# Optimization experiments

Hardware: AMD Instinct MI355X
Metric: run time of the kernel (lower is better)

The kernel has to match this reference:

```python
import jax, jax.numpy as jnp
import numpy as np

DIM = 2048
N_HEADS = 16
Q_LORA = 1536
KV_LORA = 512
NOPE = 128
ROPE = 64
QK_D = NOPE + ROPE  # 192
V_D = 128
EPS = 1e-6
B, S = 2, 2048


def rmsnorm(x, w, eps=EPS):
    return x * jax.lax.rsqrt(jnp.mean(x * x, axis=-1, keepdims=True) + eps) * w


def rotate_pe(x, cos, sin):
    # x: [B, S, H, ROPE]; cos/sin: [S, ROPE] -> broadcast [1, S, 1, ROPE]
    c = cos[None, :, None, :]
    s = sin[None, :, None, :]
    x1, x2 = jnp.split(x, 2, axis=-1)
    rot = jnp.concatenate([-x2, x1], axis=-1)
    return x * c + rot * s


def setup_inputs() -> dict:
    key = jax.random.key(0)
    ks = jax.random.split(key, 8)
    std = 0.02
    x = jax.random.normal(ks[0], (B, S, DIM), dtype=jnp.float32)
    # proper rotary tables
    inv_freq = 1.0 / (10000.0 ** (np.arange(0, ROPE, 2, dtype=np.float32) / ROPE))
    t = np.arange(S, dtype=np.float32)
    freqs = np.outer(t, inv_freq)  # [S, ROPE/2]
    emb = np.concatenate([freqs, freqs], axis=-1)  # [S, ROPE]
    cos = jnp.asarray(np.cos(emb))
    sin = jnp.asarray(np.sin(emb))
    wq_a = jax.random.normal(ks[1], (Q_LORA, DIM), dtype=jnp.float32) * std
    q_norm_w = jnp.ones((Q_LORA,), dtype=jnp.float32)
    wq_b = jax.random.normal(ks[2], (N_HEADS * QK_D, Q_LORA), dtype=jnp.float32) * std
    wkv_a = jax.random.normal(ks[3], (KV_LORA + ROPE, DIM), dtype=jnp.float32) * std
    kv_norm_w = jnp.ones((KV_LORA,), dtype=jnp.float32)
    wkv_b = jax.random.normal(ks[4], (N_HEADS * (NOPE + V_D), KV_LORA), dtype=jnp.float32) * std
    wo = jax.random.normal(ks[5], (DIM, N_HEADS * V_D), dtype=jnp.float32) * std
    return {"x": x, "cos": cos, "sin": sin, "wq_a": wq_a, "q_norm_w": q_norm_w,
            "wq_b": wq_b, "wkv_a": wkv_a, "kv_norm_w": kv_norm_w, "wkv_b": wkv_b, "wo": wo}


def mla_forward(x, cos, sin, wq_a, q_norm_w, wq_b, wkv_a, kv_norm_w, wkv_b, wo):
    bsz, seqlen, _ = x.shape
    scale = QK_D ** (-0.5)
    # Q path: low-rank down-proj -> RMSNorm -> up-proj
    q = rmsnorm(x @ wq_a.T, q_norm_w) @ wq_b.T
    q = q.reshape(bsz, seqlen, N_HEADS, QK_D)
    q_nope, q_pe = q[..., :NOPE], q[..., NOPE:]
    q_pe = rotate_pe(q_pe, cos, sin)
    q = jnp.concatenate([q_nope, q_pe], axis=-1)
    # KV path: shared low-rank latent + single rope slice
    kv = x @ wkv_a.T  # [B, S, KV_LORA + ROPE]
    kv_c, k_pe = kv[..., :KV_LORA], kv[..., KV_LORA:]
    k_pe = rotate_pe(k_pe[:, :, None, :], cos, sin)  # [B, S, 1, ROPE]
    kvb = rmsnorm(kv_c, kv_norm_w) @ wkv_b.T
    kvb = kvb.reshape(bsz, seqlen, N_HEADS, NOPE + V_D)
    k_nope, v = kvb[..., :NOPE], kvb[..., NOPE:]
    k = jnp.concatenate([k_nope, jnp.broadcast_to(k_pe, (bsz, seqlen, N_HEADS, ROPE))], axis=-1)
    # causal attention
    scores = jnp.einsum('bqhd,bkhd->bhqk', q, k) * scale
    mask = jnp.tril(jnp.ones((seqlen, seqlen), dtype=bool))
    scores = jnp.where(mask[None, None], scores, jnp.finfo(scores.dtype).min)
    p = jax.nn.softmax(scores, axis=-1)
    out = jnp.einsum('bhqk,bkhd->bqhd', p, v)
    out = out.reshape(bsz, seqlen, N_HEADS * V_D)
    return out @ wo.T


def reference(x, cos, sin, wq_a, q_norm_w, wq_b, wkv_a, kv_norm_w, wkv_b, wo):
    return mla_forward(x, cos, sin, wq_a, q_norm_w, wq_b, wkv_a, kv_norm_w, wkv_b, wo)
```

## Files before the change

kernel.cpp:

```cpp
#include <hip/hip_runtime.h>

typedef unsigned short u16;
typedef __attribute__((ext_vector_type(8))) short short8;
typedef __attribute__((ext_vector_type(4))) float floatx4;

__device__ __forceinline__ float bf2f(u16 u) {
  union { unsigned int i; float f; } v; v.i = ((unsigned int)u) << 16; return v.f;
}
__device__ __forceinline__ u16 f2bf(float f) {
  union { float f; unsigned int i; } v; v.f = f;
  unsigned int u = v.i;
  u += 0x7fffu + ((u >> 16) & 1u);
  return (u16)(u >> 16);
}

__device__ __forceinline__ void gld_lds16(const void* g, void* l) {
  __builtin_amdgcn_global_load_lds(
      (const __attribute__((address_space(1))) unsigned int*)g,
      (__attribute__((address_space(3))) unsigned int*)l, 16, 0, 0);
}

#define SBAR()   __builtin_amdgcn_s_barrier()
#define SCHED0() __builtin_amdgcn_sched_barrier(0)

__global__ __launch_bounds__(256) void repack_all_k(
    const float* __restrict__ x, const float* __restrict__ wqa,
    const float* __restrict__ wkva, const float* __restrict__ wqb,
    const float* __restrict__ wkvb, const float* __restrict__ wo,
    u16* __restrict__ xb, u16* __restrict__ wcat, u16* __restrict__ wqbb,
    u16* __restrict__ wkbb, u16* __restrict__ wob) {
  long i = ((long)blockIdx.x * 256 + threadIdx.x) * 4;
  int region = blockIdx.y;
  const float* s = nullptr; u16* d = nullptr; long n = 0;
  switch (region) {
    case 0: s = x;    d = xb;   n = 4096L * 2048; break;
    case 1: s = nullptr; d = wcat; n = 2304L * 2048; break;
    case 2: s = wqb;  d = wqbb; n = 3072L * 1536; break;
    case 3: s = wkvb; d = wkbb; n = 4096L * 512;  break;
    case 4: s = wo;   d = wob;  n = 2048L * 2048; break;
  }
  if (i >= n) return;
  float4 v;
  if (region == 1) {
    long r = i >> 11, c = i & 2047;
    if (r < 1536)      v = *(const float4*)(wqa + r * 2048 + c);
    else if (r < 2112) v = *(const float4*)(wkva + (r - 1536) * 2048 + c);
    else               v = (float4){0.f, 0.f, 0.f, 0.f};
  } else {
    v = *(const float4*)(s + i);
  }
  d[i + 0] = f2bf(v.x); d[i + 1] = f2bf(v.y);
  d[i + 2] = f2bf(v.z); d[i + 3] = f2bf(v.w);
}

#define GPHASE(LAc, LBc, QQ, STAGE_STMT, WAIT_STMT)                              \
  {                                                                              \
    short8 a00 = *(const short8*)&(LAc)[agbase + (2*(QQ)) * 1024 + g0];          \
    short8 a01 = *(const short8*)&(LAc)[agbase + (2*(QQ)) * 1024 + g1];          \
    short8 a10 = *(const short8*)&(LAc)[agbase + (2*(QQ)+1) * 1024 + g0];        \
    short8 a11 = *(const short8*)&(LAc)[agbase + (2*(QQ)+1) * 1024 + g1];        \
    if ((QQ) == 0) {                                                             \
      _Pragma("unroll")                                                          \
      for (int fj = 0; fj < 4; ++fj) {                                           \
        bfrg[fj][0] = *(const short8*)&(LBc)[bgbase + fj * 1024 + g0];           \
        bfrg[fj][1] = *(const short8*)&(LBc)[bgbase + fj * 1024 + g1];           \
      }                                                                          \
    }                                                                            \
    STAGE_STMT;                                                                  \
    WAIT_STMT;                                                                   \
    SCHED0();                                                                    \
    SBAR();                                                                      \
    asm volatile("s_waitcnt lgkmcnt(0)" ::: "memory");                           \
    SCHED0();                                                                    \
    __builtin_amdgcn_s_setprio(1);                                               \
    _Pragma("unroll")                                                            \
    for (int fj = 0; fj < 4; ++fj) {                                             \
      acc[2*(QQ)][fj]   = __builtin_amdgcn_mfma_f32_16x16x32_bf16(a00, bfrg[fj][0], acc[2*(QQ)][fj],   0, 0, 0); \
      acc[2*(QQ)][fj]   = __builtin_amdgcn_mfma_f32_16x16x32_bf16(a01, bfrg[fj][1], acc[2*(QQ)][fj],   0, 0, 0); \
      acc[2*(QQ)+1][fj] = __builtin_amdgcn_mfma_f32_16x16x32_bf16(a10, bfrg[fj][0], acc[2*(QQ)+1][fj], 0, 0, 0); \
      acc[2*(QQ)+1][fj] = __builtin_amdgcn_mfma_f32_16x16x32_bf16(a11, bfrg[fj][1], acc[2*(QQ)+1][fj], 0, 0, 0); \
    }                                                                            \
    __builtin_amdgcn_s_setprio(0);                                               \
    SCHED0();                                                                    \
    SBAR();                                                                      \
  }

template <int OUT_F32, int ROPE>
__device__ __forceinline__ void gemm256_tile(
    const u16* __restrict__ A, int lda, const u16* __restrict__ W, int ldw,
    void* __restrict__ Cv, int ldc, int K, int bm, int bn,
    u16* __restrict__ LA, u16* __restrict__ LB,
    const float* __restrict__ cosb, const float* __restrict__ sinb, int smask) {
  int tid = threadIdx.x;
  int lane = tid & 63, w = tid >> 6;
  int wr = w >> 2, wc = w & 3;
  int fr = lane & 15, fq = lane >> 4;

  int srow = lane >> 3;
  int sgl  = (lane & 7) ^ srow;

  int agbase = (wr * 128 + fr) * 64;
  int bgbase = (wc * 64 + fr) * 64;
  int g0 = ((0 * 4 + fq) ^ (fr & 7)) * 8;
  int g1 = ((1 * 4 + fq) ^ (fr & 7)) * 8;

  floatx4 acc[8][4];
#pragma unroll
  for (int i = 0; i < 8; i++)
#pragma unroll
    for (int j = 0; j < 4; j++) acc[i][j] = (floatx4){0.f, 0.f, 0.f, 0.f};

  auto stA = [&](int buf, int kt, int half) {
#pragma unroll
    for (int j = 0; j < 2; ++j) {
      int rbase = half * 128 + (w * 2 + j) * 8;
      gld_lds16(A + (size_t)(bm + rbase + srow) * lda + kt * 64 + sgl * 8,
                (void*)&LA[buf * 16384 + rbase * 64]);
    }
  };
  auto stB = [&](int buf, int kt, int half) {
#pragma unroll
    for (int j = 0; j < 2; ++j) {
      int rbase = half * 128 + (w * 2 + j) * 8;
      gld_lds16(W + (size_t)(bn + rbase + srow) * ldw + kt * 64 + sgl * 8,
                (void*)&LB[buf * 16384 + rbase * 64]);
    }
  };

  const u16* LA0 = LA;           const u16* LB0 = LB;
  const u16* LA1 = LA + 16384;   const u16* LB1 = LB + 16384;

  stB(0, 0, 0); stB(0, 0, 1);
  stA(0, 0, 0); stA(0, 0, 1);
  stB(1, 1, 0); stB(1, 1, 1);
  asm volatile("s_waitcnt vmcnt(4)" ::: "memory");
  SCHED0();
  SBAR();

  int NI = K >> 7;
  for (int i = 0; i < NI; ++i) {
    bool notlast = (i + 1 < NI);
    int t0 = 2 * i;
    {
      short8 bfrg[4][2];
      GPHASE(LA0, LB0, 0, stA(1, t0 + 1, 0), );
      GPHASE(LA0, LB0, 1, stA(1, t0 + 1, 1), );
      GPHASE(LA0, LB0, 2, if (notlast) stB(0, t0 + 2, 0), );
      GPHASE(LA0, LB0, 3, if (notlast) stB(0, t0 + 2, 1),
             if (notlast) { asm volatile("s_waitcnt vmcnt(4)" ::: "memory"); }
             else         { asm volatile("s_waitcnt vmcnt(0)" ::: "memory"); });
    }
    {
      short8 bfrg[4][2];
      GPHASE(LA1, LB1, 0, if (notlast) stA(0, t0 + 2, 0), );
      GPHASE(LA1, LB1, 1, if (notlast) stA(0, t0 + 2, 1), );
      GPHASE(LA1, LB1, 2, if (notlast) stB(1, t0 + 3, 0), );
      GPHASE(LA1, LB1, 3, if (notlast) stB(1, t0 + 3, 1),
             if (notlast) { asm volatile("s_waitcnt vmcnt(4)" ::: "memory"); });
    }
  }

  int cr = (lane >> 4) * 4, cc = lane & 15;

  if (ROPE) {
    int cw = (bn + wc * 64) >> 6;
    if (cw % 3 == 2) {
#pragma unroll
      for (int fi = 0; fi < 8; ++fi)
#pragma unroll
        for (int r = 0; r < 4; ++r) {
          int row = bm + wr * 128 + fi * 16 + cr + r;
          int pos = row & smask;
          const float* cb = cosb + pos * 64;
          const float* sb = sinb + pos * 64;
#pragma unroll
          for (int fj = 0; fj < 2; ++fj) {
            int i1 = fj * 16 + cc;
            float x1 = acc[fi][fj][r], x2 = acc[fi][fj + 2][r];
            acc[fi][fj][r]     = x1 * cb[i1] - x2 * sb[i1];
            acc[fi][fj + 2][r] = x2 * cb[i1 + 32] + x1 * sb[i1 + 32];
          }
        }
    }
  }

#pragma unroll
  for (int fi = 0; fi < 8; ++fi)
#pragma unroll
    for (int fj = 0; fj < 4; ++fj) {
      int col = bn + wc * 64 + fj * 16 + cc;
#pragma unroll
      for (int r = 0; r < 4; ++r) {
        size_t row = (size_t)(bm + wr * 128 + fi * 16 + cr + r);
        if (OUT_F32) ((float*)Cv)[row * ldc + col] = acc[fi][fj][r];
        else         ((u16*)Cv)[row * ldc + col] = f2bf(acc[fi][fj][r]);
      }
    }
}

template <int OUT_F32>
__global__ __launch_bounds__(512, 2) void gemm256_k(
    const u16* __restrict__ A, int lda,
    const u16* __restrict__ W, int ldw,
    void* __restrict__ Cv, int ldc, int K) {
  __shared__ __align__(16) u16 LAs[2][256 * 64];
  __shared__ __align__(16) u16 LBs[2][256 * 64];
  gemm256_tile<OUT_F32, 0>(A, lda, W, ldw, Cv, ldc, K,
                           blockIdx.y * 256, blockIdx.x * 256,
                           &LAs[0][0], &LBs[0][0], nullptr, nullptr, 0);
}

__global__ __launch_bounds__(512, 2) void gemm256_dual(
    const u16* __restrict__ A1, int lda1, const u16* __restrict__ W1, int ldw1,
    u16* __restrict__ C1, int ldc1, int K1, int nt1,
    const u16* __restrict__ A2, int lda2, const u16* __restrict__ W2, int ldw2,
    u16* __restrict__ C2, int ldc2, int K2,
    const float* __restrict__ cosb, const float* __restrict__ sinb, int smask) {
  __shared__ __align__(16) u16 LAs[2][256 * 64];
  __shared__ __align__(16) u16 LBs[2][256 * 64];
  int bx = blockIdx.x;
  if (bx < nt1)
    gemm256_tile<0, 1>(A1, lda1, W1, ldw1, C1, ldc1, K1,
                       blockIdx.y * 256, bx * 256, &LAs[0][0], &LBs[0][0],
                       cosb, sinb, smask);
  else
    gemm256_tile<0, 0>(A2, lda2, W2, ldw2, C2, ldc2, K2,
                       blockIdx.y * 256, (bx - nt1) * 256, &LAs[0][0], &LBs[0][0],
                       nullptr, nullptr, 0);
}

__global__ __launch_bounds__(256) void normrope_k(
    u16* __restrict__ qkv, const float* __restrict__ qnw,
    const float* __restrict__ kvnw, const float* __restrict__ cosb,
    const float* __restrict__ sinb, int S) {
  int row = blockIdx.x, tid = threadIdx.x;
  u16* p = qkv + (size_t)row * 2304;
  float s1 = 0.f, s2 = 0.f;
#pragma unroll
  for (int it = 0; it < 6; it++) { float v = bf2f(p[tid + 256 * it]); s1 += v * v; }
#pragma unroll
  for (int it = 0; it < 2; it++) { float v = bf2f(p[1536 + tid + 256 * it]); s2 += v * v; }
  for (int off = 32; off > 0; off >>= 1) {
    s1 += __shfl_down(s1, off);
    s2 += __shfl_down(s2, off);
  }
  __shared__ float red1[4], red2[4];
  if ((tid & 63) == 0) { red1[tid >> 6] = s1; red2[tid >> 6] = s2; }
  __syncthreads();
  float inv1 = rsqrtf((red1[0] + red1[1] + red1[2] + red1[3]) / 1536.f + 1e-6f);
  float inv2 = rsqrtf((red2[0] + red2[1] + red2[2] + red2[3]) / 512.f + 1e-6f);
#pragma unroll
  for (int it = 0; it < 6; it++) {
    int i = tid + 256 * it;
    p[i] = f2bf(bf2f(p[i]) * inv1 * qnw[i]);
  }
#pragma unroll
  for (int it = 0; it < 2; it++) {
    int i = tid + 256 * it;
    p[1536 + i] = f2bf(bf2f(p[1536 + i]) * inv2 * kvnw[i]);
  }
  if (tid < 32) {
    int pos = row % S;
    float c1 = cosb[pos * 64 + tid];
    float c2 = cosb[pos * 64 + tid + 32];
    float sn1 = sinb[pos * 64 + tid];
    float sn2 = sinb[pos * 64 + tid + 32];
    float x1 = bf2f(p[2048 + tid]), x2 = bf2f(p[2048 + tid + 32]);
    p[2048 + tid]      = f2bf(x1 * c1 - x2 * sn1);
    p[2048 + tid + 32] = f2bf(x2 * c2 + x1 * sn2);
  }
}

__global__ __launch_bounds__(256) void vtrans_k(
    const u16* __restrict__ kvb, u16* __restrict__ vt, int S) {
  int tb = blockIdx.x, h = blockIdx.y, b = blockIdx.z;
  __shared__ __align__(16) u16 Ts[64][136];
  int tid = threadIdx.x;
#pragma unroll
  for (int it = 0; it < 4; it++) {
    int e = tid + 256 * it;
    int tok = e >> 4, c = e & 15;
    short8 v = *(const short8*)(kvb + (size_t)(b * S + tb * 64 + tok) * 4096 + h * 256 + 128 + c * 8);
    *(short8*)&Ts[tok][c * 8] = v;
  }
  __syncthreads();
  int vd = tid >> 1, half = (tid & 1) * 32;
  u16 tmp[32];
#pragma unroll
  for (int j = 0; j < 32; j++) tmp[j] = Ts[half + j][vd];
  u16* dst = vt + ((size_t)((b * 16 + h) * 128) + vd) * S + tb * 64 + half;
#pragma unroll
  for (int c = 0; c < 4; c++)
    *(short8*)(dst + c * 8) = *(short8*)&tmp[c * 8];
}

#define AT_BK 64
__global__ __launch_bounds__(256) void attn_mfma(
    const u16* __restrict__ qf, const u16* __restrict__ kvb,
    const u16* __restrict__ kpe, int kpe_stride, const u16* __restrict__ vt,
    u16* __restrict__ at, int S) {
  int id = blockIdx.x;
  int pair = id >> 5, hb = id & 31;
  int h = hb & 15, b = hb >> 4;
  int NT = S / AT_BK;
  int tid = threadIdx.x, lane = tid & 63, w = tid >> 6;
  int fr = lane & 15, fq = lane >> 4;
  int fs = fr & 7;

  __shared__ __align__(16) u16 Ksn[AT_BK * 128];
  __shared__ __align__(16) u16 Ksp[AT_BK * 64];
  __shared__ __align__(16) u16 Vts[128 * AT_BK];
  __shared__ __align__(16) u16 Ps[64 * AT_BK];

  const float scale = 0.07216878364870323f;

  for (int p = 0; p < 2; p++) {
    int qt = p ? (NT - 1 - pair) : pair;
    int q0 = qt * 64;

    short8 qfrag[6];
    {
      const u16* qrow = qf + (size_t)(b * S + q0 + w * 16 + fr) * 3072 + h * 192 + fq * 8;
#pragma unroll
      for (int ks = 0; ks < 6; ks++) qfrag[ks] = *(const short8*)(qrow + ks * 32);
    }

    floatx4 acc_o[8];
#pragma unroll
    for (int j = 0; j < 8; j++) acc_o[j] = (floatx4){0.f, 0.f, 0.f, 0.f};
    float m_r[4], l_r[4];
#pragma unroll
    for (int r = 0; r < 4; r++) { m_r[r] = -3e38f; l_r[r] = 0.f; }

    for (int kt = 0; kt <= qt; kt++) {
      int k0 = kt * AT_BK;
      size_t tokbase = (size_t)(b * S + k0);
#pragma unroll
      for (int c = 0; c < 4; c++) {
        int row = w * 16 + c * 4 + (lane >> 4);
        int cg = (lane & 15) ^ (row & 7);
        gld_lds16(kvb + (tokbase + row) * 4096 + h * 256 + cg * 8,
                  &Ksn[(w * 16 + c * 4) * 128]);
      }
#pragma unroll
      for (int c = 0; c < 2; c++) {
        int row = w * 16 + c * 8 + (lane >> 3);
        int cg = (lane & 7) ^ (row & 7);
        gld_lds16(kpe + (tokbase + row) * kpe_stride + cg * 8,
                  &Ksp[(w * 16 + c * 8) * 64]);
      }
#pragma unroll
      for (int c = 0; c < 4; c++) {
        int vd = w * 32 + c * 8 + (lane >> 3);
        int cg = (lane & 7) ^ (vd & 7);
        gld_lds16(vt + ((size_t)((b * 16 + h) * 128) + vd) * S + k0 + cg * 8,
                  &Vts[(w * 32 + c * 8) * 64]);
      }
      __syncthreads();

      floatx4 accs[4];
#pragma unroll
      for (int nt = 0; nt < 4; nt++) accs[nt] = (floatx4){0.f, 0.f, 0.f, 0.f};
      __builtin_amdgcn_s_setprio(1);
#pragma unroll
      for (int nt = 0; nt < 4; nt++) {
#pragma unroll
        for (int ks = 0; ks < 4; ks++) {
          short8 bf = *(const short8*)&Ksn[(nt * 16 + fr) * 128 + ((ks * 4 + fq) ^ fs) * 8];
          accs[nt] = __builtin_amdgcn_mfma_f32_16x16x32_bf16(qfrag[ks], bf, accs[nt], 0, 0, 0);
        }
#pragma unroll
        for (int ks = 0; ks < 2; ks++) {
          short8 bf = *(const short8*)&Ksp[(nt * 16 + fr) * 64 + ((ks * 4 + fq) ^ fs) * 8];
          accs[nt] = __builtin_amdgcn_mfma_f32_16x16x32_bf16(qfrag[4 + ks], bf, accs[nt], 0, 0, 0);
        }
      }
      __builtin_amdgcn_s_setprio(0);

      bool diag = (kt == qt);
#pragma unroll
      for (int nt = 0; nt < 4; nt++)
#pragma unroll
        for (int r = 0; r < 4; r++) {
          float s = accs[nt][r] * scale;
          if (diag) {
            int col = nt * 16 + fr;
            int row = fq * 4 + r;
            if (k0 + col > q0 + w * 16 + row) s = -3e38f;
          }
          accs[nt][r] = s;
        }

      float mx4[4];
      int grow = 0;
#pragma unroll
      for (int r = 0; r < 4; r++) {
        float mx = fmaxf(fmaxf(accs[0][r], accs[1][r]), fmaxf(accs[2][r], accs[3][r]));
        mx = fmaxf(mx, __shfl_xor(mx, 1));
        mx = fmaxf(mx, __shfl_xor(mx, 2));
        mx = fmaxf(mx, __shfl_xor(mx, 4));
        mx = fmaxf(mx, __shfl_xor(mx, 8));
        mx4[r] = mx;
        grow |= (mx > m_r[r] + 8.f) ? 1 : 0;
      }
      bool resc = __any(grow);
      float alpha[4];
      if (resc) {
#pragma unroll
        for (int r = 0; r < 4; r++) {
          float mnew = fmaxf(m_r[r], mx4[r]);
          alpha[r] = __expf(m_r[r] - mnew);
          m_r[r] = mnew;
          l_r[r] *= alpha[r];
        }
      }
#pragma unroll
      for (int nt = 0; nt < 4; nt++)
#pragma unroll
        for (int r = 0; r < 4; r++) {
          float pv = __expf(accs[nt][r] - m_r[r]);
          l_r[r] += pv;
          int row_p = w * 16 + fq * 4 + r;
          int col = nt * 16 + fr;
          Ps[row_p * 64 + (((col >> 3) ^ (row_p & 7)) * 8) + (col & 7)] = f2bf(pv);
        }
      __syncthreads();

      if (resc) {
#pragma unroll
        for (int j = 0; j < 8; j++)
#pragma unroll
          for (int r = 0; r < 4; r++) acc_o[j][r] *= alpha[r];
      }
      short8 pf0 = *(const short8*)&Ps[(w * 16 + fr) * 64 + (fq ^ fs) * 8];
      short8 pf1 = *(const short8*)&Ps[(w * 16 + fr) * 64 + ((4 + fq) ^ fs) * 8];
      __builtin_amdgcn_s_setprio(1);
#pragma unroll
      for (int j = 0; j < 8; j++) {
        short8 v0 = *(const short8*)&Vts[(j * 16 + fr) * 64 + (fq ^ fs) * 8];
        short8 v1 = *(const short8*)&Vts[(j * 16 + fr) * 64 + ((4 + fq) ^ fs) * 8];
        acc_o[j] = __builtin_amdgcn_mfma_f32_16x16x32_bf16(pf0, v0, acc_o[j], 0, 0, 0);
        acc_o[j] = __builtin_amdgcn_mfma_f32_16x16x32_bf16(pf1, v1, acc_o[j], 0, 0, 0);
      }
      __builtin_amdgcn_s_setprio(0);
      __syncthreads();
    }

    float inv_l[4];
#pragma unroll
    for (int r = 0; r < 4; r++) {
      float sm = l_r[r];
      sm += __shfl_xor(sm, 1);
      sm += __shfl_xor(sm, 2);
      sm += __shfl_xor(sm, 4);
      sm += __shfl_xor(sm, 8);
      inv_l[r] = 1.f / sm;
    }
#pragma unroll
    for (int j = 0; j < 8; j++)
#pragma unroll
      for (int r = 0; r < 4; r++) {
        size_t row = (size_t)(b * S + q0 + w * 16 + fq * 4 + r);
        at[row * 2048 + h * 128 + j * 16 + fr] = f2bf(acc_o[j][r] * inv_l[r]);
      }
  }
}

extern "C" void kernel_launch(void* const* d_in, const int* in_sizes, int n_in,
                              void* d_out, int out_size, void* d_ws, size_t ws_size,
                              hipStream_t stream) {
  (void)in_sizes; (void)n_in; (void)out_size; (void)ws_size;
  const float* x     = (const float*)d_in[0];
  const float* cosb  = (const float*)d_in[1];
  const float* sinb  = (const float*)d_in[2];
  const float* wq_a  = (const float*)d_in[3];
  const float* qnw   = (const float*)d_in[4];
  const float* wq_b  = (const float*)d_in[5];
  const float* wkv_a = (const float*)d_in[6];
  const float* kvnw  = (const float*)d_in[7];
  const float* wkv_b = (const float*)d_in[8];
  const float* wo    = (const float*)d_in[9];
  float* out = (float*)d_out;
  const int B = 2, S = 2048, T = B * S;

  char* wsb = (char*)d_ws;
  size_t off = 0;
  u16* xb   = (u16*)(wsb + off); off += (size_t)T * 2048 * 2;
  u16* wcat = (u16*)(wsb + off); off += (size_t)2304 * 2048 * 2;
  u16* wqbb = (u16*)(wsb + off); off += (size_t)3072 * 1536 * 2;
  u16* wkbb = (u16*)(wsb + off); off += (size_t)4096 * 512 * 2;
  u16* wob  = (u16*)(wsb + off); off += (size_t)2048 * 2048 * 2;
  u16* qkv  = (u16*)(wsb + off); off += (size_t)T * 2304 * 2;
  u16* qf   = (u16*)(wsb + off); off += (size_t)T * 3072 * 2;
  u16* kvb  = (u16*)(wsb + off); off += (size_t)T * 4096 * 2;
  u16* at   = (u16*)(wsb + off); off += (size_t)T * 2048 * 2;
  u16* vt   = xb;

  repack_all_k<<<dim3(8192, 5), 256, 0, stream>>>(
      x, wq_a, wkv_a, wq_b, wkv_b, wo, xb, wcat, wqbb, wkbb, wob);

  gemm256_k<0><<<dim3(2304 / 256, T / 256), 512, 0, stream>>>(xb, 2048, wcat, 2048, qkv, 2304, 2048);
  normrope_k<<<T, 256, 0, stream>>>(qkv, qnw, kvnw, cosb, sinb, S);
  gemm256_dual<<<dim3(3072 / 256 + 4096 / 256, T / 256), 512, 0, stream>>>(
      qkv, 2304, wqbb, 1536, qf, 3072, 1536, 3072 / 256,
      qkv + 1536, 2304, wkbb, 512, kvb, 4096, 512,
      cosb, sinb, S - 1);
  vtrans_k<<<dim3(S / 64, 16, B), 256, 0, stream>>>(kvb, vt, S);
  attn_mfma<<<dim3((S / 128) * 32), 256, 0, stream>>>(qf, kvb, qkv + 2048, 2304, vt, at, S);
  gemm256_k<1><<<dim3(2048 / 256, T / 256), 512, 0, stream>>>(at, 2048, wob, 2048, out, 2048, 2048);
}
```

Measured before the change: 461.9 us.

## Use 256x128 GEMM tiles and shrink padded QKV projection width

Adds a new GEMM kernel with 256x128 output tiles and uses it for the fused Q/KV down-projection and the output projection, replacing the 256x256 kernel. The fused weight is now padded only to 2176 rows instead of 2304, which removes wasted padded columns. Narrower tiles also double the block count for the 2048-wide output GEMM, giving better CU fill on a 256-CU device. The cost is lower reuse of each A tile per block and more total loads of A.

```diff
diff --git a/kernel.cpp b/kernel.cpp
--- a/kernel.cpp
+++ b/kernel.cpp
@@ -34,7 +34,7 @@
   const float* s = nullptr; u16* d = nullptr; long n = 0;
   switch (region) {
     case 0: s = x;    d = xb;   n = 4096L * 2048; break;
-    case 1: s = nullptr; d = wcat; n = 2304L * 2048; break;
+    case 1: s = nullptr; d = wcat; n = 2176L * 2048; break;
     case 2: s = wqb;  d = wqbb; n = 3072L * 1536; break;
     case 3: s = wkvb; d = wkbb; n = 4096L * 512;  break;
     case 4: s = wo;   d = wob;  n = 2048L * 2048; break;
@@ -198,18 +198,6 @@
     }
 }
 
-template <int OUT_F32>
-__global__ __launch_bounds__(512, 2) void gemm256_k(
-    const u16* __restrict__ A, int lda,
-    const u16* __restrict__ W, int ldw,
-    void* __restrict__ Cv, int ldc, int K) {
-  __shared__ __align__(16) u16 LAs[2][256 * 64];
-  __shared__ __align__(16) u16 LBs[2][256 * 64];
-  gemm256_tile<OUT_F32, 0>(A, lda, W, ldw, Cv, ldc, K,
-                           blockIdx.y * 256, blockIdx.x * 256,
-                           &LAs[0][0], &LBs[0][0], nullptr, nullptr, 0);
-}
-
 __global__ __launch_bounds__(512, 2) void gemm256_dual(
     const u16* __restrict__ A1, int lda1, const u16* __restrict__ W1, int ldw1,
     u16* __restrict__ C1, int ldc1, int K1, int nt1,
@@ -229,12 +217,133 @@
                        nullptr, nullptr, 0);
 }
 
+#define GPHASE128(LAc, LBc, QQ, STAGE_STMT, WAIT_STMT)                           \
+  {                                                                              \
+    short8 a00 = *(const short8*)&(LAc)[agbase + (2*(QQ)) * 1024 + g0];          \
+    short8 a01 = *(const short8*)&(LAc)[agbase + (2*(QQ)) * 1024 + g1];          \
+    short8 a10 = *(const short8*)&(LAc)[agbase + (2*(QQ)+1) * 1024 + g0];        \
+    short8 a11 = *(const short8*)&(LAc)[agbase + (2*(QQ)+1) * 1024 + g1];        \
+    if ((QQ) == 0) {                                                             \
+      _Pragma("unroll")                                                          \
+      for (int fj = 0; fj < 2; ++fj) {                                           \
+        bfrg[fj][0] = *(const short8*)&(LBc)[bgbase + fj * 1024 + g0];           \
+        bfrg[fj][1] = *(const short8*)&(LBc)[bgbase + fj * 1024 + g1];           \
+      }                                                                          \
+    }                                                                            \
+    STAGE_STMT;                                                                  \
+    WAIT_STMT;                                                                   \
+    SCHED0();                                                                    \
+    SBAR();                                                                      \
+    asm volatile("s_waitcnt lgkmcnt(0)" ::: "memory");                           \
+    SCHED0();                                                                    \
+    __builtin_amdgcn_s_setprio(1);                                               \
+    _Pragma("unroll")                                                            \
+    for (int fj = 0; fj < 2; ++fj) {                                             \
+      acc[2*(QQ)][fj]   = __builtin_amdgcn_mfma_f32_16x16x32_bf16(a00, bfrg[fj][0], acc[2*(QQ)][fj],   0, 0, 0); \
+      acc[2*(QQ)][fj]   = __builtin_amdgcn_mfma_f32_16x16x32_bf16(a01, bfrg[fj][1], acc[2*(QQ)][fj],   0, 0, 0); \
+      acc[2*(QQ)+1][fj] = __builtin_amdgcn_mfma_f32_16x16x32_bf16(a10, bfrg[fj][0], acc[2*(QQ)+1][fj], 0, 0, 0); \
+      acc[2*(QQ)+1][fj] = __builtin_amdgcn_mfma_f32_16x16x32_bf16(a11, bfrg[fj][1], acc[2*(QQ)+1][fj], 0, 0, 0); \
+    }                                                                            \
+    __builtin_amdgcn_s_setprio(0);                                               \
+    SCHED0();                                                                    \
+    SBAR();                                                                      \
+  }
+
+template <int OUT_F32>
+__global__ __launch_bounds__(512, 2) void gemm128n_k(
+    const u16* __restrict__ A, int lda,
+    const u16* __restrict__ W, int ldw,
+    void* __restrict__ Cv, int ldc, int K) {
+  __shared__ __align__(16) u16 LA[2][256 * 64];
+  __shared__ __align__(16) u16 LB[2][128 * 64];
+  int bm = blockIdx.y * 256, bn = blockIdx.x * 128;
+  int tid = threadIdx.x;
+  int lane = tid & 63, w = tid >> 6;
+  int wr = w >> 2, wc = w & 3;
+  int fr = lane & 15, fq = lane >> 4;
+
+  int srow = lane >> 3;
+  int sgl  = (lane & 7) ^ srow;
+
+  int agbase = (wr * 128 + fr) * 64;
+  int bgbase = (wc * 32 + fr) * 64;
+  int g0 = ((0 * 4 + fq) ^ (fr & 7)) * 8;
+  int g1 = ((1 * 4 + fq) ^ (fr & 7)) * 8;
+
+  floatx4 acc[8][2];
+#pragma unroll
+  for (int i = 0; i < 8; i++)
+#pragma unroll
+    for (int j = 0; j < 2; j++) acc[i][j] = (floatx4){0.f, 0.f, 0.f, 0.f};
+
+  auto stA = [&](int buf, int kt, int half) {
+#pragma unroll
+    for (int j = 0; j < 2; ++j) {
+      int rbase = half * 128 + (w * 2 + j) * 8;
+      gld_lds16(A + (size_t)(bm + rbase + srow) * lda + kt * 64 + sgl * 8,
+                (void*)&LA[buf][rbase * 64]);
+    }
+  };
+  auto stB = [&](int buf, int kt, int half) {
+    int rbase = half * 64 + w * 8;
+    gld_lds16(W + (size_t)(bn + rbase + srow) * ldw + kt * 64 + sgl * 8,
+              (void*)&LB[buf][rbase * 64]);
+  };
+
+  const u16* LA0 = &LA[0][0];  const u16* LB0 = &LB[0][0];
+  const u16* LA1 = &LA[1][0];  const u16* LB1 = &LB[1][0];
+
+  stB(0, 0, 0); stB(0, 0, 1);
+  stA(0, 0, 0); stA(0, 0, 1);
+  stB(1, 1, 0); stB(1, 1, 1);
+  asm volatile("s_waitcnt vmcnt(2)" ::: "memory");
+  SCHED0();
+  SBAR();
+
+  int NI = K >> 7;
+  for (int i = 0; i < NI; ++i) {
+    bool notlast = (i + 1 < NI);
+    int t0 = 2 * i;
+    {
+      short8 bfrg[2][2];
+      GPHASE128(LA0, LB0, 0, stA(1, t0 + 1, 0), );
+      GPHASE128(LA0, LB0, 1, stA(1, t0 + 1, 1), );
+      GPHASE128(LA0, LB0, 2, if (notlast) stB(0, t0 + 2, 0), );
+      GPHASE128(LA0, LB0, 3, if (notlast) stB(0, t0 + 2, 1),
+             if (notlast) { asm volatile("s_waitcnt vmcnt(2)" ::: "memory"); }
+             else         { asm volatile("s_waitcnt vmcnt(0)" ::: "memory"); });
+    }
+    {
+      short8 bfrg[2][2];
+      GPHASE128(LA1, LB1, 0, if (notlast) stA(0, t0 + 2, 0), );
+      GPHASE128(LA1, LB1, 1, if (notlast) stA(0, t0 + 2, 1), );
+      GPHASE128(LA1, LB1, 2, if (notlast) stB(1, t0 + 3, 0), );
+      GPHASE128(LA1, LB1, 3, if (notlast) stB(1, t0 + 3, 1),
+             if (notlast) { asm volatile("s_waitcnt vmcnt(2)" ::: "memory"); });
+    }
+  }
+
+  int cr = (lane >> 4) * 4, cc = lane & 15;
+#pragma unroll
+  for (int fi = 0; fi < 8; ++fi)
+#pragma unroll
+    for (int fj = 0; fj < 2; ++fj) {
+      int col = bn + wc * 32 + fj * 16 + cc;
+#pragma unroll
+      for (int r = 0; r < 4; ++r) {
+        size_t row = (size_t)(bm + wr * 128 + fi * 16 + cr + r);
+        if (OUT_F32) ((float*)Cv)[row * ldc + col] = acc[fi][fj][r];
+        else         ((u16*)Cv)[row * ldc + col] = f2bf(acc[fi][fj][r]);
+      }
+    }
+}
+
 __global__ __launch_bounds__(256) void normrope_k(
     u16* __restrict__ qkv, const float* __restrict__ qnw,
     const float* __restrict__ kvnw, const float* __restrict__ cosb,
     const float* __restrict__ sinb, int S) {
   int row = blockIdx.x, tid = threadIdx.x;
-  u16* p = qkv + (size_t)row * 2304;
+  u16* p = qkv + (size_t)row * 2176;
   float s1 = 0.f, s2 = 0.f;
 #pragma unroll
   for (int it = 0; it < 6; it++) { float v = bf2f(p[tid + 256 * it]); s1 += v * v; }
@@ -486,11 +595,11 @@
   char* wsb = (char*)d_ws;
   size_t off = 0;
   u16* xb   = (u16*)(wsb + off); off += (size_t)T * 2048 * 2;
-  u16* wcat = (u16*)(wsb + off); off += (size_t)2304 * 2048 * 2;
+  u16* wcat = (u16*)(wsb + off); off += (size_t)2176 * 2048 * 2;
   u16* wqbb = (u16*)(wsb + off); off += (size_t)3072 * 1536 * 2;
   u16* wkbb = (u16*)(wsb + off); off += (size_t)4096 * 512 * 2;
   u16* wob  = (u16*)(wsb + off); off += (size_t)2048 * 2048 * 2;
-  u16* qkv  = (u16*)(wsb + off); off += (size_t)T * 2304 * 2;
+  u16* qkv  = (u16*)(wsb + off); off += (size_t)T * 2176 * 2;
   u16* qf   = (u16*)(wsb + off); off += (size_t)T * 3072 * 2;
   u16* kvb  = (u16*)(wsb + off); off += (size_t)T * 4096 * 2;
   u16* at   = (u16*)(wsb + off); off += (size_t)T * 2048 * 2;
@@ -499,13 +608,13 @@
   repack_all_k<<<dim3(8192, 5), 256, 0, stream>>>(
       x, wq_a, wkv_a, wq_b, wkv_b, wo, xb, wcat, wqbb, wkbb, wob);
 
-  gemm256_k<0><<<dim3(2304 / 256, T / 256), 512, 0, stream>>>(xb, 2048, wcat, 2048, qkv, 2304, 2048);
+  gemm128n_k<0><<<dim3(2176 / 128, T / 256), 512, 0, stream>>>(xb, 2048, wcat, 2048, qkv, 2176, 2048);
   normrope_k<<<T, 256, 0, stream>>>(qkv, qnw, kvnw, cosb, sinb, S);
   gemm256_dual<<<dim3(3072 / 256 + 4096 / 256, T / 256), 512, 0, stream>>>(
-      qkv, 2304, wqbb, 1536, qf, 3072, 1536, 3072 / 256,
-      qkv + 1536, 2304, wkbb, 512, kvb, 4096, 512,
+      qkv, 2176, wqbb, 1536, qf, 3072, 1536, 3072 / 256,
+      qkv + 1536, 2176, wkbb, 512, kvb, 4096, 512,
       cosb, sinb, S - 1);
   vtrans_k<<<dim3(S / 64, 16, B), 256, 0, stream>>>(kvb, vt, S);
-  attn_mfma<<<dim3((S / 128) * 32), 256, 0, stream>>>(qf, kvb, qkv + 2048, 2304, vt, at, S);
-  gemm256_k<1><<<dim3(2048 / 256, T / 256), 512, 0, stream>>>(at, 2048, wob, 2048, out, 2048, 2048);
-}
+  attn_mfma<<<dim3((S / 128) * 32), 256, 0, stream>>>(qf, kvb, qkv + 2048, 2176, vt, at, S);
+  gemm128n_k<1><<<dim3(2048 / 128, T / 256), 512, 0, stream>>>(at, 2048, wob, 2048, out, 2048, 2048);
+}
```

Result: no change. 465.2 us (+0.7%).
